# Optimization experiments

Measured on AMD Instinct MI355X. Metric: run time of the kernel, lower is better.

## Reference

```python
import jax, jax.numpy as jnp
import numpy as np

EPS = 1e-6
H = 12  # num_attention_heads

def _phi(x):
    # feature map used by fast-transformers LinearAttention: elu(x) + 1
    return jax.nn.elu(x) + 1.0

def setup_inputs() -> dict:
    key = jax.random.key(0)
    k1, k2, k3 = jax.random.split(key, 3)
    B, N, D = 32, 1024, 768
    x = jax.random.normal(k1, (B, N, D), dtype=jnp.float32)
    W_qkv = jax.random.normal(k2, (D, 3 * D), dtype=jnp.float32) * (D ** -0.5)
    W_out = jax.random.normal(k3, (D, D), dtype=jnp.float32) * (D ** -0.5)
    b_out = jnp.zeros((D,), dtype=jnp.float32)
    return {"x": x, "W_qkv": W_qkv, "W_out": W_out, "b_out": b_out}

def reference(x, W_qkv, W_out, b_out):
    B, N, D = x.shape
    d = D // H
    # F.pad(x, [0,0,0,1]): append one zero token along sequence
    x_ = jnp.pad(x, ((0, 0), (0, 1), (0, 0)))              # [B, N+1, D]
    qkv = x_ @ W_qkv                                        # [B, N+1, 3D]
    q, k, v = jnp.split(qkv, 3, axis=-1)
    q = q.reshape(B, N + 1, H, d)
    k = k.reshape(B, N + 1, H, d)
    v = v.reshape(B, N + 1, H, d)
    # non-causal linear attention (mask is all-ones -> no masking)
    q = _phi(q)
    k = _phi(k)
    kv = jnp.einsum('bshd,bshm->bhdm', k, v)                # [B, H, d, d]
    z = 1.0 / (jnp.einsum('blhd,bhd->blh', q, k.sum(axis=1)) + EPS)
    out = jnp.einsum('blhd,bhdm,blh->blhm', q, kv, z)       # [B, N+1, H, d]
    out = out.reshape(B, N + 1, D)
    out = out @ W_out + b_out                               # dropout = identity (eval)
    return out[:, :-1, :]                                   # drop padding token
```

## Files before the change

### kernel.cpp

```cpp
#include <hip/hip_runtime.h>
#include <hip/hip_bf16.h>


typedef __bf16 bf16x8 __attribute__((ext_vector_type(8)));
typedef float f32x4 __attribute__((ext_vector_type(4)));

__device__ __forceinline__ ushort f2bf(float f) {
  union { float f; unsigned u; } x; x.f = f;
  unsigned r = x.u + 0x7fffu + ((x.u >> 16) & 1u);
  return (ushort)(r >> 16);
}
__device__ __forceinline__ float bf2f(ushort h) {
  union { unsigned u; float f; } x; x.u = ((unsigned)h) << 16;
  return x.f;
}
__device__ __forceinline__ void gload_lds16(const void* g, void* lds) {
  __builtin_amdgcn_global_load_lds((const __attribute__((address_space(1))) void*)g,
                                   (__attribute__((address_space(3))) void*)lds, 16, 0, 0);
}

__global__ __launch_bounds__(256) void cvt_f32_bf16(const float* __restrict__ in,
                                                    ushort* __restrict__ out, int n4) {
  int i = blockIdx.x * 256 + threadIdx.x;
  if (i >= n4) return;
  float4 v = reinterpret_cast<const float4*>(in)[i];
  ushort4 o;
  o.x = f2bf(v.x); o.y = f2bf(v.y); o.z = f2bf(v.z); o.w = f2bf(v.w);
  reinterpret_cast<ushort4*>(out)[i] = o;
}

__global__ __launch_bounds__(256) void transpose_cvt(const float* __restrict__ src,
                                                     ushort* __restrict__ dst, int R, int C) {
  __shared__ float tile[32][33];
  int bc = blockIdx.x * 32, br = blockIdx.y * 32;
  int tx = threadIdx.x & 31, ty = threadIdx.x >> 5;
  #pragma unroll
  for (int i = 0; i < 32; i += 8)
    tile[ty + i][tx] = src[(size_t)(br + ty + i) * C + (bc + tx)];
  __syncthreads();
  #pragma unroll
  for (int i = 0; i < 32; i += 8)
    dst[(size_t)(bc + ty + i) * R + (br + tx)] = f2bf(tile[tx][ty + i]);
}

template <int MODE>
__global__ __launch_bounds__(512, 2) void gemm256(const ushort* __restrict__ A,
                                                  const ushort* __restrict__ Bt,
                                                  void* __restrict__ C,
                                                  const float* __restrict__ bias,
                                                  int N, int K, int nbx, int cpx) {
  extern __shared__ ushort lds[];
  const int tid = threadIdx.x;
  const int lane = tid & 63;
  const int wid = tid >> 6;
  const int wm = wid >> 2, wn = wid & 3;
  const int laneR = lane & 15, laneS = lane >> 4;

  const int bid = blockIdx.x;
  const int lin = (bid & 7) * cpx + (bid >> 3);
  const int by = lin / nbx, bx = lin - by * nbx;
  const int m0 = by * 256, n0 = bx * 256;
  const int NT = K >> 6;

  const int sr = tid >> 2, ss = tid & 3;
  const int sslot = ss ^ ((sr >> 1) & 3);
  const ushort* Asrc0 = A + (size_t)(m0 + sr) * K + sslot * 8;
  const ushort* Bsrc0 = Bt + (size_t)(n0 + sr) * K + sslot * 8;
  const size_t rowstep = (size_t)128 * K;
  const int ldst0 = tid * 8;

  const int sprime = laneS ^ ((laneR >> 1) & 3);
  const int aoff = (wm * 128 + laneR) * 32 + sprime * 8;
  const int boff = 16384 + (wn * 64 + laneR) * 32 + sprime * 8;

  f32x4 acc[8][4] = {};
  bf16x8 afrX[4], afrY[4], bfrX[4], bfrY[4];

  #define STAGE_HT(SRC, KT, KS, DST)                                              \
    { gload_lds16((SRC) + (KT) * 64 + (KS) * 32,                                  \
                  (DST) + (KS) * 8192 + ldst0);                                   \
      gload_lds16((SRC) + (KT) * 64 + (KS) * 32 + rowstep,                        \
                  (DST) + (KS) * 8192 + 4096 + ldst0); }
  #define SBAR  __builtin_amdgcn_sched_barrier(0)
  #define MFMA16(ACCBASE, AF, BF)                                                 \
    _Pragma("unroll")                                                             \
    for (int ii = 0; ii < 4; ++ii)                                                \
      _Pragma("unroll")                                                           \
      for (int j = 0; j < 4; ++j)                                                 \
        acc[(ACCBASE) + ii][j] =                                                  \
            __builtin_amdgcn_mfma_f32_16x16x32_bf16(AF[ii], BF[j], acc[(ACCBASE) + ii][j], 0, 0, 0);

  {
    ushort* b0 = lds;
    ushort* b1 = lds + 32768;
    STAGE_HT(Asrc0, 0, 0, b0);
    STAGE_HT(Bsrc0, 0, 0, b0 + 16384);
    STAGE_HT(Asrc0, 0, 1, b0);
    STAGE_HT(Bsrc0, 0, 1, b0 + 16384);
    STAGE_HT(Asrc0, 1, 0, b1);
    STAGE_HT(Bsrc0, 1, 0, b1 + 16384);
  }
  asm volatile("s_waitcnt vmcnt(8)" ::: "memory");
  SBAR;
  __builtin_amdgcn_s_barrier();
  SBAR;
  #pragma unroll
  for (int j = 0; j < 4; ++j)
    bfrX[j] = *(const bf16x8*)(lds + boff + j * 512);
  #pragma unroll
  for (int ii = 0; ii < 4; ++ii)
    afrX[ii] = *(const bf16x8*)(lds + aoff + ii * 512);

  for (int t = 0; t < NT; ++t) {
    ushort* cbuf = lds + (t & 1) * 32768;
    ushort* nbuf = lds + ((t & 1) ^ 1) * 32768;
    const int t1 = (t + 1 < NT) ? t + 1 : t;
    const int t2 = (t + 2 < NT) ? t + 2 : t;

    STAGE_HT(Asrc0, t1, 1, nbuf);
    asm volatile("s_waitcnt vmcnt(6)" ::: "memory");
    SBAR;
    #pragma unroll
    for (int ii = 0; ii < 4; ++ii)
      afrY[ii] = *(const bf16x8*)(cbuf + aoff + (4 + ii) * 512);
    SBAR;
    __builtin_amdgcn_s_setprio(1);
    MFMA16(0, afrX, bfrX);
    __builtin_amdgcn_s_setprio(0);
    SBAR;
    __builtin_amdgcn_s_barrier();
    SBAR;

    STAGE_HT(Bsrc0, t1, 1, nbuf + 16384);
    SBAR;
    #pragma unroll
    for (int j = 0; j < 4; ++j)
      bfrY[j] = *(const bf16x8*)(cbuf + 8192 + boff + j * 512);
    #pragma unroll
    for (int ii = 0; ii < 4; ++ii)
      afrX[ii] = *(const bf16x8*)(cbuf + 8192 + aoff + ii * 512);
    SBAR;
    __builtin_amdgcn_s_setprio(1);
    MFMA16(4, afrY, bfrX);
    __builtin_amdgcn_s_setprio(0);
    SBAR;
    __builtin_amdgcn_s_barrier();
    SBAR;

    STAGE_HT(Asrc0, t2, 0, cbuf);
    asm volatile("s_waitcnt vmcnt(6)" ::: "memory");
    SBAR;
    #pragma unroll
    for (int ii = 0; ii < 4; ++ii)
      afrY[ii] = *(const bf16x8*)(cbuf + 8192 + aoff + (4 + ii) * 512);
    SBAR;
    __builtin_amdgcn_s_setprio(1);
    MFMA16(0, afrX, bfrY);
    __builtin_amdgcn_s_setprio(0);
    SBAR;
    __builtin_amdgcn_s_barrier();
    SBAR;

    STAGE_HT(Bsrc0, t2, 0, cbuf + 16384);
    SBAR;
    #pragma unroll
    for (int j = 0; j < 4; ++j)
      bfrX[j] = *(const bf16x8*)(nbuf + boff + j * 512);
    #pragma unroll
    for (int ii = 0; ii < 4; ++ii)
      afrX[ii] = *(const bf16x8*)(nbuf + aoff + ii * 512);
    SBAR;
    __builtin_amdgcn_s_setprio(1);
    MFMA16(4, afrY, bfrY);
    __builtin_amdgcn_s_setprio(0);
    SBAR;
    __builtin_amdgcn_s_barrier();
    SBAR;
  }
  #undef STAGE_HT
  #undef MFMA16
  asm volatile("s_waitcnt vmcnt(0)" ::: "memory");

  #pragma unroll
  for (int i = 0; i < 8; ++i) {
    const int grow0 = m0 + wm * 128 + i * 16 + (laneS << 2);
    #pragma unroll
    for (int j = 0; j < 4; ++j) {
      const int gcol = n0 + wn * 64 + j * 16 + laneR;
      #pragma unroll
      for (int r = 0; r < 4; ++r) {
        float v = acc[i][j][r];
        if (MODE == 0) {
          if (gcol < 1536) v = (v > 0.f) ? (v + 1.f) : __expf(v);
          reinterpret_cast<ushort*>(C)[(size_t)(grow0 + r) * N + gcol] = f2bf(v);
        } else {
          reinterpret_cast<float*>(C)[(size_t)(grow0 + r) * N + gcol] = v + bias[gcol];
        }
      }
    }
  }
}

__global__ __launch_bounds__(256) void kv_partial(const ushort* __restrict__ qkv,
                                                  float* __restrict__ kv_part,
                                                  float* __restrict__ ks_part) {
  const int blk = blockIdx.x;
  const int bh = blk >> 2, sp = blk & 3;
  const int b = bh / 12, h = bh % 12;
  const int tid = threadIdx.x;
  __shared__ ushort Ks[32 * 64];
  __shared__ ushort Vs[32 * 64];
  float acc[4][4] = {};
  float kacc[4] = {};
  const int dq0 = (tid & 15) * 4, mq0 = (tid >> 4) * 4;
  const int r = tid >> 3, o = tid & 7;
  for (int st = 0; st < 256; st += 32) {
    const int s0 = sp * 256 + st;
    __syncthreads();
    const size_t rowbase = (size_t)(b * 1024 + s0 + r) * 2304 + h * 64 + o * 8;
    gload_lds16(qkv + rowbase + 768,  &Ks[tid * 8]);
    gload_lds16(qkv + rowbase + 1536, &Vs[tid * 8]);
    asm volatile("s_waitcnt vmcnt(0)" ::: "memory");
    __syncthreads();
    #pragma unroll 8
    for (int s = 0; s < 32; ++s) {
      short4 kk = *reinterpret_cast<const short4*>(&Ks[s * 64 + dq0]);
      short4 vv = *reinterpret_cast<const short4*>(&Vs[s * 64 + mq0]);
      float kf[4] = { bf2f((ushort)kk.x), bf2f((ushort)kk.y), bf2f((ushort)kk.z), bf2f((ushort)kk.w) };
      float vf[4] = { bf2f((ushort)vv.x), bf2f((ushort)vv.y), bf2f((ushort)vv.z), bf2f((ushort)vv.w) };
      #pragma unroll
      for (int jm = 0; jm < 4; ++jm)
        #pragma unroll
        for (int id = 0; id < 4; ++id)
          acc[jm][id] += vf[jm] * kf[id];
      if (mq0 == 0) {
        #pragma unroll
        for (int id = 0; id < 4; ++id) kacc[id] += kf[id];
      }
    }
  }
  float* kvp = kv_part + ((size_t)sp * 384 + bh) * 4096;
  #pragma unroll
  for (int jm = 0; jm < 4; ++jm)
    #pragma unroll
    for (int id = 0; id < 4; ++id)
      kvp[(mq0 + jm) * 64 + dq0 + id] = acc[jm][id];
  if (mq0 == 0) {
    #pragma unroll
    for (int id = 0; id < 4; ++id)
      ks_part[((size_t)sp * 384 + bh) * 64 + dq0 + id] = kacc[id];
  }
}

__global__ __launch_bounds__(256) void kv_reduce(const float* __restrict__ kv_part,
                                                 const float* __restrict__ ks_part,
                                                 ushort* __restrict__ kv_bf,
                                                 float* __restrict__ ksum) {
  int i = blockIdx.x * 256 + threadIdx.x;
  if (i < 384 * 4096) {
    float s = 0.f;
    #pragma unroll
    for (int p = 0; p < 4; ++p) s += kv_part[(size_t)p * (384 * 4096) + i];
    kv_bf[i] = f2bf(s);
  }
  if (i < 384 * 64) {
    float s = 1.0f;
    #pragma unroll
    for (int p = 0; p < 4; ++p) s += ks_part[(size_t)p * (384 * 64) + i];
    ksum[i] = s;
  }
}

__global__ __launch_bounds__(256) void attn_kernel(const ushort* __restrict__ qkv,
                                                   const ushort* __restrict__ kv_bf,
                                                   const float* __restrict__ ksum,
                                                   ushort* __restrict__ attn) {
  const int blk = blockIdx.x;
  const int bh = blk >> 3, tb = blk & 7;
  const int b = bh / 12, h = bh % 12;
  const int row0 = b * 1024 + tb * 128;
  __shared__ ushort Qs[128 * 64];
  __shared__ ushort KVs[64 * 64];
  __shared__ float zs[128];
  __shared__ float ks_lds[64];
  const int tid = threadIdx.x;
  const int lane = tid & 63, w = tid >> 6;
  #pragma unroll
  for (int j = 0; j < 4; ++j) {
    int c = j * 256 + tid;
    gload_lds16(qkv + (size_t)(row0 + (c >> 3)) * 2304 + h * 64 + (c & 7) * 8, &Qs[c * 8]);
  }
  #pragma unroll
  for (int j = 0; j < 2; ++j) {
    int c = j * 256 + tid;
    gload_lds16(kv_bf + (size_t)bh * 4096 + c * 8, &KVs[c * 8]);
  }
  if (tid < 64) ks_lds[tid] = ksum[bh * 64 + tid];
  asm volatile("s_waitcnt vmcnt(0)" ::: "memory");
  __syncthreads();
  if (tid < 128) {
    float d = 0.f;
    #pragma unroll 8
    for (int e = 0; e < 64; ++e) d += bf2f(Qs[tid * 64 + e]) * ks_lds[e];
    zs[tid] = 1.f / (d + 1e-6f);
  }
  __syncthreads();
  f32x4 acc[2][4] = {};
  #pragma unroll
  for (int ks = 0; ks < 2; ++ks) {
    bf16x8 a[2], bb[4];
    #pragma unroll
    for (int i = 0; i < 2; ++i)
      a[i] = *reinterpret_cast<const bf16x8*>(&Qs[(w * 32 + i * 16 + (lane & 15)) * 64 + ks * 32 + (lane >> 4) * 8]);
    #pragma unroll
    for (int j = 0; j < 4; ++j)
      bb[j] = *reinterpret_cast<const bf16x8*>(&KVs[(j * 16 + (lane & 15)) * 64 + ks * 32 + (lane >> 4) * 8]);
    #pragma unroll
    for (int i = 0; i < 2; ++i)
      #pragma unroll
      for (int j = 0; j < 4; ++j)
        acc[i][j] = __builtin_amdgcn_mfma_f32_16x16x32_bf16(a[i], bb[j], acc[i][j], 0, 0, 0);
  }
  #pragma unroll
  for (int i = 0; i < 2; ++i) {
    const int t0 = w * 32 + i * 16 + ((lane >> 4) << 2);
    #pragma unroll
    for (int j = 0; j < 4; ++j) {
      const int m = j * 16 + (lane & 15);
      #pragma unroll
      for (int r = 0; r < 4; ++r) {
        float v = acc[i][j][r] * zs[t0 + r];
        attn[(size_t)(row0 + t0 + r) * 768 + h * 64 + m] = f2bf(v);
      }
    }
  }
}

extern "C" void kernel_launch(void* const* d_in, const int* in_sizes, int n_in,
                              void* d_out, int out_size, void* d_ws, size_t ws_size,
                              hipStream_t stream) {
  (void)in_sizes; (void)n_in; (void)out_size; (void)ws_size;
  const float* x    = (const float*)d_in[0];
  const float* Wqkv = (const float*)d_in[1];
  const float* Wout = (const float*)d_in[2];
  const float* bout = (const float*)d_in[3];
  float* out = (float*)d_out;
  char* ws = (char*)d_ws;

  ushort* xbf    = (ushort*)(ws);
  ushort* wqkvT  = (ushort*)(ws + 50331648);
  ushort* woutT  = (ushort*)(ws + 53870592);
  ushort* qkv    = (ushort*)(ws + 55050240);
  float*  ksp    = (float*) (ws + 206045184);
  ushort* kvbf   = (ushort*)(ws + 206438400);
  float*  ksum   = (float*) (ws + 209584128);
  float*  kvpart = (float*)(ws);
  ushort* attn   = (ushort*)(ws);

  static const int LDS_BYTES = 131072;
  hipFuncSetAttribute(reinterpret_cast<const void*>(&gemm256<0>),
                      hipFuncAttributeMaxDynamicSharedMemorySize, LDS_BYTES);
  hipFuncSetAttribute(reinterpret_cast<const void*>(&gemm256<1>),
                      hipFuncAttributeMaxDynamicSharedMemorySize, LDS_BYTES);

  cvt_f32_bf16<<<24576, 256, 0, stream>>>(x, xbf, 6291456);
  transpose_cvt<<<dim3(72, 24), 256, 0, stream>>>(Wqkv, wqkvT, 768, 2304);
  transpose_cvt<<<dim3(24, 24), 256, 0, stream>>>(Wout, woutT, 768, 768);
  gemm256<0><<<1152, 512, LDS_BYTES, stream>>>(xbf, wqkvT, qkv, nullptr, 2304, 768, 9, 144);
  kv_partial<<<1536, 256, 0, stream>>>(qkv, kvpart, ksp);
  kv_reduce<<<6144, 256, 0, stream>>>(kvpart, ksp, kvbf, ksum);
  attn_kernel<<<3072, 256, 0, stream>>>(qkv, kvbf, ksum, attn);
  gemm256<1><<<384, 512, LDS_BYTES, stream>>>(attn, woutT, out, bout, 768, 768, 3, 48);
}
```

Measured before the change: 315.6 us.

## Replace register double-buffered fragments with single-buffer inline-asm LDS reads per phase

Removes the X/Y register double-buffering of A/B fragments in the GEMM main loop. Each phase now issues its LDS reads through inline ds_read_b128 asm together with the global-to-LDS prefetch, then waits on lgkmcnt(0) after a barrier before running the MFMAs. This cuts fragment register pressure and simplifies scheduling. In exchange, LDS read latency is no longer hidden behind the previous phase's MFMAs, and the volatile asm constrains compiler scheduling.

```diff
diff --git a/kernel.cpp b/kernel.cpp
--- a/kernel.cpp
+++ b/kernel.cpp
@@ -17,6 +17,13 @@
 __device__ __forceinline__ void gload_lds16(const void* g, void* lds) {
   __builtin_amdgcn_global_load_lds((const __attribute__((address_space(1))) void*)g,
                                    (__attribute__((address_space(3))) void*)lds, 16, 0, 0);
+}
+__device__ __forceinline__ bf16x8 ds_read128(const ushort* p) {
+  bf16x8 r;
+  asm volatile("ds_read_b128 %0, %1"
+               : "=v"(r)
+               : "v"((const __attribute__((address_space(3))) ushort*)p));
+  return r;
 }
 
 __global__ __launch_bounds__(256) void cvt_f32_bf16(const float* __restrict__ in,
@@ -74,7 +81,7 @@
   const int boff = 16384 + (wn * 64 + laneR) * 32 + sprime * 8;
 
   f32x4 acc[8][4] = {};
-  bf16x8 afrX[4], afrY[4], bfrX[4], bfrY[4];
+  bf16x8 afr[4], bfr[4];
 
   #define STAGE_HT(SRC, KT, KS, DST)                                              \
     { gload_lds16((SRC) + (KT) * 64 + (KS) * 32,                                  \
@@ -82,13 +89,24 @@
       gload_lds16((SRC) + (KT) * 64 + (KS) * 32 + rowstep,                        \
                   (DST) + (KS) * 8192 + 4096 + ldst0); }
   #define SBAR  __builtin_amdgcn_sched_barrier(0)
-  #define MFMA16(ACCBASE, AF, BF)                                                 \
+  #define PHASE_SYNC                                                              \
+    SBAR;                                                                         \
+    __builtin_amdgcn_s_barrier();                                                 \
+    asm volatile("s_waitcnt lgkmcnt(0)");                                         \
+    SBAR;
+  #define PHASE_END                                                               \
+    SBAR;                                                                         \
+    __builtin_amdgcn_s_barrier();                                                 \
+    SBAR;
+  #define MFMA16(ACCBASE)                                                         \
+    __builtin_amdgcn_s_setprio(1);                                                \
     _Pragma("unroll")                                                             \
     for (int ii = 0; ii < 4; ++ii)                                                \
       _Pragma("unroll")                                                           \
       for (int j = 0; j < 4; ++j)                                                 \
         acc[(ACCBASE) + ii][j] =                                                  \
-            __builtin_amdgcn_mfma_f32_16x16x32_bf16(AF[ii], BF[j], acc[(ACCBASE) + ii][j], 0, 0, 0);
+            __builtin_amdgcn_mfma_f32_16x16x32_bf16(afr[ii], bfr[j], acc[(ACCBASE) + ii][j], 0, 0, 0); \
+    __builtin_amdgcn_s_setprio(0);
 
   {
     ushort* b0 = lds;
@@ -104,12 +122,6 @@
   SBAR;
   __builtin_amdgcn_s_barrier();
   SBAR;
-  #pragma unroll
-  for (int j = 0; j < 4; ++j)
-    bfrX[j] = *(const bf16x8*)(lds + boff + j * 512);
-  #pragma unroll
-  for (int ii = 0; ii < 4; ++ii)
-    afrX[ii] = *(const bf16x8*)(lds + aoff + ii * 512);
 
   for (int t = 0; t < NT; ++t) {
     ushort* cbuf = lds + (t & 1) * 32768;
@@ -117,68 +129,44 @@
     const int t1 = (t + 1 < NT) ? t + 1 : t;
     const int t2 = (t + 2 < NT) ? t + 2 : t;
 
+    #pragma unroll
+    for (int j = 0; j < 4; ++j) bfr[j] = ds_read128(cbuf + boff + j * 512);
+    #pragma unroll
+    for (int ii = 0; ii < 4; ++ii) afr[ii] = ds_read128(cbuf + aoff + ii * 512);
     STAGE_HT(Asrc0, t1, 1, nbuf);
     asm volatile("s_waitcnt vmcnt(6)" ::: "memory");
-    SBAR;
-    #pragma unroll
-    for (int ii = 0; ii < 4; ++ii)
-      afrY[ii] = *(const bf16x8*)(cbuf + aoff + (4 + ii) * 512);
-    SBAR;
-    __builtin_amdgcn_s_setprio(1);
-    MFMA16(0, afrX, bfrX);
-    __builtin_amdgcn_s_setprio(0);
-    SBAR;
-    __builtin_amdgcn_s_barrier();
-    SBAR;
-
+    PHASE_SYNC;
+    MFMA16(0);
+    PHASE_END;
+
+    #pragma unroll
+    for (int ii = 0; ii < 4; ++ii) afr[ii] = ds_read128(cbuf + aoff + (4 + ii) * 512);
     STAGE_HT(Bsrc0, t1, 1, nbuf + 16384);
-    SBAR;
-    #pragma unroll
-    for (int j = 0; j < 4; ++j)
-      bfrY[j] = *(const bf16x8*)(cbuf + 8192 + boff + j * 512);
-    #pragma unroll
-    for (int ii = 0; ii < 4; ++ii)
-      afrX[ii] = *(const bf16x8*)(cbuf + 8192 + aoff + ii * 512);
-    SBAR;
-    __builtin_amdgcn_s_setprio(1);
-    MFMA16(4, afrY, bfrX);
-    __builtin_amdgcn_s_setprio(0);
-    SBAR;
-    __builtin_amdgcn_s_barrier();
-    SBAR;
-
+    PHASE_SYNC;
+    MFMA16(4);
+    PHASE_END;
+
+    #pragma unroll
+    for (int j = 0; j < 4; ++j) bfr[j] = ds_read128(cbuf + 8192 + boff + j * 512);
+    #pragma unroll
+    for (int ii = 0; ii < 4; ++ii) afr[ii] = ds_read128(cbuf + 8192 + aoff + ii * 512);
     STAGE_HT(Asrc0, t2, 0, cbuf);
     asm volatile("s_waitcnt vmcnt(6)" ::: "memory");
-    SBAR;
-    #pragma unroll
-    for (int ii = 0; ii < 4; ++ii)
-      afrY[ii] = *(const bf16x8*)(cbuf + 8192 + aoff + (4 + ii) * 512);
-    SBAR;
-    __builtin_amdgcn_s_setprio(1);
-    MFMA16(0, afrX, bfrY);
-    __builtin_amdgcn_s_setprio(0);
-    SBAR;
-    __builtin_amdgcn_s_barrier();
-    SBAR;
-
+    PHASE_SYNC;
+    MFMA16(0);
+    PHASE_END;
+
+    #pragma unroll
+    for (int ii = 0; ii < 4; ++ii) afr[ii] = ds_read128(cbuf + 8192 + aoff + (4 + ii) * 512);
     STAGE_HT(Bsrc0, t2, 0, cbuf + 16384);
-    SBAR;
-    #pragma unroll
-    for (int j = 0; j < 4; ++j)
-      bfrX[j] = *(const bf16x8*)(nbuf + boff + j * 512);
-    #pragma unroll
-    for (int ii = 0; ii < 4; ++ii)
-      afrX[ii] = *(const bf16x8*)(nbuf + aoff + ii * 512);
-    SBAR;
-    __builtin_amdgcn_s_setprio(1);
-    MFMA16(4, afrY, bfrY);
-    __builtin_amdgcn_s_setprio(0);
-    SBAR;
-    __builtin_amdgcn_s_barrier();
-    SBAR;
+    PHASE_SYNC;
+    MFMA16(4);
+    PHASE_END;
   }
   #undef STAGE_HT
   #undef MFMA16
+  #undef PHASE_SYNC
+  #undef PHASE_END
   asm volatile("s_waitcnt vmcnt(0)" ::: "memory");
 
   #pragma unroll
```

Measured after the change: 318.1 us. About the same (+0.8%).

## Add two-phase pipelined GEMM for output projection and fp32 LDS in kv_partial

Applied to the files above, without the earlier changes.

Adds a new gemm2ph kernel with 128-row tiles, a two-phase split of each K tile with double-buffered async global-to-LDS loads, and explicit barriers and priority around MFMA clusters. It replaces the output-projection GEMM, doubling the grid to 768 blocks and allowing two blocks per CU via smaller LDS. Separately, kv_partial now loads K/V through registers, converts bf16 to fp32 once, and stores padded fp32 rows in LDS, removing repeated per-inner-loop conversions and bank conflicts. The cost is more LDS traffic in kv_partial and new hand-scheduled code paths that must hold up correctness.

```diff
diff --git a/kernel.cpp b/kernel.cpp
--- a/kernel.cpp
+++ b/kernel.cpp
@@ -14,9 +14,20 @@
   union { unsigned u; float f; } x; x.u = ((unsigned)h) << 16;
   return x.f;
 }
+__device__ __forceinline__ float bits2f(unsigned u) {
+  union { unsigned u; float f; } x; x.u = u;
+  return x.f;
+}
 __device__ __forceinline__ void gload_lds16(const void* g, void* lds) {
   __builtin_amdgcn_global_load_lds((const __attribute__((address_space(1))) void*)g,
                                    (__attribute__((address_space(3))) void*)lds, 16, 0, 0);
+}
+__device__ __forceinline__ bf16x8 ds_read128(const ushort* p) {
+  bf16x8 r;
+  asm volatile("ds_read_b128 %0, %1"
+               : "=v"(r)
+               : "v"((const __attribute__((address_space(3))) ushort*)p));
+  return r;
 }
 
 __global__ __launch_bounds__(256) void cvt_f32_bf16(const float* __restrict__ in,
@@ -201,6 +212,137 @@
   }
 }
 
+template <int MODE, int MFR>
+__global__ __launch_bounds__(512, 2) void gemm2ph(const ushort* __restrict__ A,
+                                                  const ushort* __restrict__ Bt,
+                                                  void* __restrict__ C,
+                                                  const float* __restrict__ bias,
+                                                  int N, int K, int nbx, int cpx) {
+  constexpr int BM   = MFR * 32;
+  constexpr int ALD  = MFR / 4;
+  constexpr int AKS  = BM * 32;
+  constexpr int BBASE = BM * 64;
+  constexpr int BUFS = (BM + 256) * 64;
+  extern __shared__ ushort lds[];
+  const int tid = threadIdx.x;
+  const int lane = tid & 63;
+  const int wid = tid >> 6;
+  const int wm = wid >> 2, wn = wid & 3;
+  const int laneR = lane & 15, laneS = lane >> 4;
+
+  const int bid = blockIdx.x;
+  const int lin = (bid & 7) * cpx + (bid >> 3);
+  const int by = lin / nbx, bx = lin - by * nbx;
+  const int m0 = by * BM, n0 = bx * 256;
+  const int NT = K >> 6;
+
+  const int sr = tid >> 2, ss = tid & 3;
+  const int sslot = ss ^ ((sr >> 1) & 3);
+  const ushort* Asrc0 = A + (size_t)(m0 + sr) * K + sslot * 8;
+  const ushort* Bsrc0 = Bt + (size_t)(n0 + sr) * K + sslot * 8;
+  const size_t rowstep = (size_t)128 * K;
+  const int ldst0 = tid * 8;
+
+  const int sprime = laneS ^ ((laneR >> 1) & 3);
+  const int aoff = (wm * (MFR * 16) + laneR) * 32 + sprime * 8;
+  const int boff = BBASE + (wn * 64 + laneR) * 32 + sprime * 8;
+
+  f32x4 acc[MFR][4] = {};
+  bf16x8 afr[MFR], bfr[4];
+
+  #define STAGE_K(KT, KS, DB)                                                     \
+    { _Pragma("unroll")                                                           \
+      for (int L = 0; L < ALD; ++L)                                               \
+        gload_lds16(Asrc0 + (KT) * 64 + (KS) * 32 + (size_t)L * rowstep,          \
+                    lds + (DB) + (KS) * AKS + L * 4096 + ldst0);                  \
+      _Pragma("unroll")                                                           \
+      for (int L = 0; L < 2; ++L)                                                 \
+        gload_lds16(Bsrc0 + (KT) * 64 + (KS) * 32 + (size_t)L * rowstep,          \
+                    lds + (DB) + BBASE + (KS) * 8192 + L * 4096 + ldst0); }
+  #define SBAR  __builtin_amdgcn_sched_barrier(0)
+  #define VMCNT_WAIT                                                              \
+    if constexpr (MFR == 8) asm volatile("s_waitcnt vmcnt(8)" ::: "memory");      \
+    else                    asm volatile("s_waitcnt vmcnt(6)" ::: "memory");
+  #define PHASE_SYNC                                                              \
+    SBAR;                                                                         \
+    __builtin_amdgcn_s_barrier();                                                 \
+    asm volatile("s_waitcnt lgkmcnt(0)");                                         \
+    SBAR;
+  #define PHASE_END                                                               \
+    SBAR;                                                                         \
+    __builtin_amdgcn_s_barrier();                                                 \
+    SBAR;
+  #define MFMA_CL                                                                 \
+    __builtin_amdgcn_s_setprio(1);                                                \
+    _Pragma("unroll")                                                             \
+    for (int ii = 0; ii < MFR; ++ii)                                              \
+      _Pragma("unroll")                                                           \
+      for (int j = 0; j < 4; ++j)                                                 \
+        acc[ii][j] =                                                              \
+            __builtin_amdgcn_mfma_f32_16x16x32_bf16(afr[ii], bfr[j], acc[ii][j], 0, 0, 0); \
+    __builtin_amdgcn_s_setprio(0);
+
+  STAGE_K(0, 0, 0);
+  STAGE_K(0, 1, 0);
+  STAGE_K(1, 0, BUFS);
+  VMCNT_WAIT;
+  SBAR;
+  __builtin_amdgcn_s_barrier();
+  SBAR;
+
+  for (int t = 0; t < NT; ++t) {
+    const int cb = (t & 1) * BUFS;
+    const int nb = BUFS - cb;
+    const int t1 = (t + 1 < NT) ? t + 1 : t;
+    const int t2 = (t + 2 < NT) ? t + 2 : t;
+
+    #pragma unroll
+    for (int j = 0; j < 4; ++j) bfr[j] = ds_read128(lds + cb + boff + j * 512);
+    #pragma unroll
+    for (int ii = 0; ii < MFR; ++ii) afr[ii] = ds_read128(lds + cb + aoff + ii * 512);
+    STAGE_K(t1, 1, nb);
+    VMCNT_WAIT;
+    PHASE_SYNC;
+    MFMA_CL;
+    PHASE_END;
+
+    #pragma unroll
+    for (int j = 0; j < 4; ++j) bfr[j] = ds_read128(lds + cb + 8192 + boff + j * 512);
+    #pragma unroll
+    for (int ii = 0; ii < MFR; ++ii) afr[ii] = ds_read128(lds + cb + AKS + aoff + ii * 512);
+    STAGE_K(t2, 0, cb);
+    VMCNT_WAIT;
+    PHASE_SYNC;
+    MFMA_CL;
+    PHASE_END;
+  }
+  #undef STAGE_K
+  #undef MFMA_CL
+  #undef PHASE_SYNC
+  #undef PHASE_END
+  #undef VMCNT_WAIT
+  asm volatile("s_waitcnt vmcnt(0)" ::: "memory");
+
+  #pragma unroll
+  for (int i = 0; i < MFR; ++i) {
+    const int grow0 = m0 + wm * (MFR * 16) + i * 16 + (laneS << 2);
+    #pragma unroll
+    for (int j = 0; j < 4; ++j) {
+      const int gcol = n0 + wn * 64 + j * 16 + laneR;
+      #pragma unroll
+      for (int r = 0; r < 4; ++r) {
+        float v = acc[i][j][r];
+        if (MODE == 0) {
+          if (gcol < 1536) v = (v > 0.f) ? (v + 1.f) : __expf(v);
+          reinterpret_cast<ushort*>(C)[(size_t)(grow0 + r) * N + gcol] = f2bf(v);
+        } else {
+          reinterpret_cast<float*>(C)[(size_t)(grow0 + r) * N + gcol] = v + bias[gcol];
+        }
+      }
+    }
+  }
+}
+
 __global__ __launch_bounds__(256) void kv_partial(const ushort* __restrict__ qkv,
                                                   float* __restrict__ kv_part,
                                                   float* __restrict__ ks_part) {
@@ -208,34 +350,47 @@
   const int bh = blk >> 2, sp = blk & 3;
   const int b = bh / 12, h = bh % 12;
   const int tid = threadIdx.x;
-  __shared__ ushort Ks[32 * 64];
-  __shared__ ushort Vs[32 * 64];
+  __shared__ float Ks[32 * 68];
+  __shared__ float Vs[32 * 68];
   float acc[4][4] = {};
   float kacc[4] = {};
   const int dq0 = (tid & 15) * 4, mq0 = (tid >> 4) * 4;
-  const int r = tid >> 3, o = tid & 7;
+  const int r = tid >> 3, o = (tid & 7) * 8;
   for (int st = 0; st < 256; st += 32) {
-    const int s0 = sp * 256 + st;
+    const size_t rowbase = (size_t)(b * 1024 + sp * 256 + st + r) * 2304 + h * 64 + o;
+    int4 kraw = *reinterpret_cast<const int4*>(qkv + rowbase + 768);
+    int4 vraw = *reinterpret_cast<const int4*>(qkv + rowbase + 1536);
+    float kf[8], vf[8];
+    {
+      const unsigned* kw = reinterpret_cast<const unsigned*>(&kraw);
+      const unsigned* vw = reinterpret_cast<const unsigned*>(&vraw);
+      #pragma unroll
+      for (int w = 0; w < 4; ++w) {
+        kf[2 * w]     = bits2f(kw[w] << 16);
+        kf[2 * w + 1] = bits2f(kw[w] & 0xffff0000u);
+        vf[2 * w]     = bits2f(vw[w] << 16);
+        vf[2 * w + 1] = bits2f(vw[w] & 0xffff0000u);
+      }
+    }
     __syncthreads();
-    const size_t rowbase = (size_t)(b * 1024 + s0 + r) * 2304 + h * 64 + o * 8;
-    gload_lds16(qkv + rowbase + 768,  &Ks[tid * 8]);
-    gload_lds16(qkv + rowbase + 1536, &Vs[tid * 8]);
-    asm volatile("s_waitcnt vmcnt(0)" ::: "memory");
+    #pragma unroll
+    for (int w = 0; w < 8; ++w) {
+      Ks[r * 68 + o + w] = kf[w];
+      Vs[r * 68 + o + w] = vf[w];
+    }
     __syncthreads();
     #pragma unroll 8
     for (int s = 0; s < 32; ++s) {
-      short4 kk = *reinterpret_cast<const short4*>(&Ks[s * 64 + dq0]);
-      short4 vv = *reinterpret_cast<const short4*>(&Vs[s * 64 + mq0]);
-      float kf[4] = { bf2f((ushort)kk.x), bf2f((ushort)kk.y), bf2f((ushort)kk.z), bf2f((ushort)kk.w) };
-      float vf[4] = { bf2f((ushort)vv.x), bf2f((ushort)vv.y), bf2f((ushort)vv.z), bf2f((ushort)vv.w) };
+      f32x4 kk = *reinterpret_cast<const f32x4*>(&Ks[s * 68 + dq0]);
+      f32x4 vv = *reinterpret_cast<const f32x4*>(&Vs[s * 68 + mq0]);
       #pragma unroll
       for (int jm = 0; jm < 4; ++jm)
         #pragma unroll
         for (int id = 0; id < 4; ++id)
-          acc[jm][id] += vf[jm] * kf[id];
+          acc[jm][id] += vv[jm] * kk[id];
       if (mq0 == 0) {
         #pragma unroll
-        for (int id = 0; id < 4; ++id) kacc[id] += kf[id];
+        for (int id = 0; id < 4; ++id) kacc[id] += kk[id];
       }
     }
   }
@@ -357,18 +512,19 @@
   float*  kvpart = (float*)(ws);
   ushort* attn   = (ushort*)(ws);
 
-  static const int LDS_BYTES = 131072;
+  static const int LDS1 = 131072;
+  static const int LDS2 = 98304;
   hipFuncSetAttribute(reinterpret_cast<const void*>(&gemm256<0>),
-                      hipFuncAttributeMaxDynamicSharedMemorySize, LDS_BYTES);
-  hipFuncSetAttribute(reinterpret_cast<const void*>(&gemm256<1>),
-                      hipFuncAttributeMaxDynamicSharedMemorySize, LDS_BYTES);
+                      hipFuncAttributeMaxDynamicSharedMemorySize, LDS1);
+  hipFuncSetAttribute(reinterpret_cast<const void*>(&gemm2ph<1, 4>),
+                      hipFuncAttributeMaxDynamicSharedMemorySize, LDS2);
 
   cvt_f32_bf16<<<24576, 256, 0, stream>>>(x, xbf, 6291456);
   transpose_cvt<<<dim3(72, 24), 256, 0, stream>>>(Wqkv, wqkvT, 768, 2304);
   transpose_cvt<<<dim3(24, 24), 256, 0, stream>>>(Wout, woutT, 768, 768);
-  gemm256<0><<<1152, 512, LDS_BYTES, stream>>>(xbf, wqkvT, qkv, nullptr, 2304, 768, 9, 144);
+  gemm256<0><<<1152, 512, LDS1, stream>>>(xbf, wqkvT, qkv, nullptr, 2304, 768, 9, 144);
   kv_partial<<<1536, 256, 0, stream>>>(qkv, kvpart, ksp);
   kv_reduce<<<6144, 256, 0, stream>>>(kvpart, ksp, kvbf, ksum);
   attn_kernel<<<3072, 256, 0, stream>>>(qkv, kvbf, ksum, attn);
-  gemm256<1><<<384, 512, LDS_BYTES, stream>>>(attn, woutT, out, bout, 768, 768, 3, 48);
-}
+  gemm2ph<1, 4><<<768, 512, LDS2, stream>>>(attn, woutT, out, bout, 768, 768, 3, 96);
+}
```

Result: faster. 304.1 us (-3.6%).
